# Kernel tuning notes

Measured on AMD Instinct MI355X. Metric: run time of the kernel, lower is better.

Reference implementation:

```python
import jax, jax.numpy as jnp
import numpy as np

N, E = 50000, 800000
IN, HID, OUT, K = 500, 128, 128, 10
BN_EPS = 1e-5


def _encode(x, src, dst, norm, n, W_in, b_in, gam, high_pass, bn_scale, bn_shift, W_up, b_up):
    # input projection (dropout_p = 0 -> identity)
    h = x @ W_in + b_in  # [N, HID]

    def prop(t):
        # symmetric-normalized sparse matvec: (D^-1/2 A D^-1/2) t
        return jax.ops.segment_sum(norm[:, None] * t[src], dst, num_segments=n)

    def step(carry, g):
        t, acc = carry
        acc = acc + g * t
        pt = prop(t)
        # low-pass basis: A_hat^k x ; high-pass basis: (I - A_hat)^k x
        t = (t - pt) if high_pass else pt
        return (t, acc), None

    (_, acc), _ = jax.lax.scan(step, (h, jnp.zeros_like(h)), gam)

    # BatchNorm1d over the node axis (training-mode batch statistics)
    mu = acc.mean(axis=0)
    var = acc.var(axis=0)
    hn = (acc - mu) * jax.lax.rsqrt(var + BN_EPS) * bn_scale + bn_shift
    z = hn @ W_up + b_up
    return jax.nn.relu(z)  # act_fn='relu' (PolyGCL default)


def setup_inputs() -> dict:
    key = jax.random.key(0)
    ks = jax.random.split(key, 4)
    x = jax.random.normal(ks[0], (N, IN), dtype=jnp.float32)
    edge_index = jax.random.randint(ks[1], (2, E), 0, N, dtype=jnp.int32)
    W_in = jax.random.normal(ks[2], (IN, HID), dtype=jnp.float32) * (1.0 / np.sqrt(IN))
    b_in = jnp.zeros((HID,), dtype=jnp.float32)
    # low-pass: decreasing coefficients; high-pass: increasing (PolyGCL init scheme)
    gamma_L = jnp.linspace(2.0, 0.0, K + 1, dtype=jnp.float32)
    gamma_H = jnp.linspace(0.0, 2.0, K + 1, dtype=jnp.float32)
    bn_scale = jnp.ones((HID,), dtype=jnp.float32)
    bn_shift = jnp.zeros((HID,), dtype=jnp.float32)
    W_up = jax.random.normal(ks[3], (HID, OUT), dtype=jnp.float32) * (1.0 / np.sqrt(HID))
    b_up = jnp.zeros((OUT,), dtype=jnp.float32)
    return {"x": x, "edge_index": edge_index, "W_in": W_in, "b_in": b_in,
            "gamma_L": gamma_L, "gamma_H": gamma_H,
            "bn_scale": bn_scale, "bn_shift": bn_shift,
            "W_up": W_up, "b_up": b_up}


def reference(x, edge_index, W_in, b_in, gamma_L, gamma_H, bn_scale, bn_shift, W_up, b_up):
    n = x.shape[0]
    src, dst = edge_index[0], edge_index[1]
    deg = jax.ops.segment_sum(jnp.ones(src.shape, dtype=x.dtype), dst, num_segments=n)
    dinv = jax.lax.rsqrt(jnp.maximum(deg, 1.0))
    norm = dinv[src] * dinv[dst]  # [E]
    Z_L = _encode(x, src, dst, norm, n, W_in, b_in, gamma_L, False, bn_scale, bn_shift, W_up, b_up)
    Z_H = _encode(x, src, dst, norm, n, W_in, b_in, gamma_H, True, bn_scale, bn_shift, W_up, b_up)
    return (Z_L, Z_H)
```

## Files before the change

kernel.cpp:

```cpp
#include <hip/hip_runtime.h>
#include <hip/hip_fp16.h>

#define HIDF 128

typedef float v4f __attribute__((ext_vector_type(4)));
typedef _Float16 half8 __attribute__((ext_vector_type(8)));
typedef float f32x4 __attribute__((ext_vector_type(4)));
struct alignas(8) half4 { __half2 lo, hi; };

static inline int cdiv(int a, int b) { return (a + b - 1) / b; }
static inline size_t alup(size_t b) { return (b + 255) & ~(size_t)255; }

__global__ void k_deg(const int* __restrict__ dst, int E, int* __restrict__ deg) {
    int i = blockIdx.x * blockDim.x + threadIdx.x;
    if (i < E) atomicAdd(&deg[dst[i]], 1);
}

__global__ void k_coef(const float* __restrict__ gL, const float* __restrict__ gH, int K,
                       float* __restrict__ cL, float* __restrict__ cH) {
    if (threadIdx.x == 0 && blockIdx.x == 0) {
        for (int j = 0; j <= K; ++j) {
            double s = 0.0;
            double C = 1.0;
            for (int k = j; k <= K; ++k) {
                s += (double)gH[k] * C;
                C = C * (double)(k + 1) / (double)(k + 1 - j);
            }
            cH[j] = (j & 1) ? (float)(-s) : (float)s;
            cL[j] = gL[j];
        }
    }
}

__global__ __launch_bounds__(256) void k_scan1(const int* __restrict__ deg, int N,
                                               int* __restrict__ bsum,
                                               float* __restrict__ dinv) {
    __shared__ int ls[256];
    int tid = threadIdx.x;
    int i = blockIdx.x * 256 + tid;
    int v = 0;
    if (i < N) {
        v = deg[i];
        dinv[i] = rsqrtf(fmaxf((float)v, 1.0f));
    }
    ls[tid] = v;
    __syncthreads();
    for (int off = 128; off > 0; off >>= 1) {
        if (tid < off) ls[tid] += ls[tid + off];
        __syncthreads();
    }
    if (tid == 0) bsum[blockIdx.x] = ls[0];
}

__global__ __launch_bounds__(1024) void k_scan2(int* __restrict__ bsum, int nb) {
    __shared__ int ls[1024];
    int tid = threadIdx.x;
    int v = (tid < nb) ? bsum[tid] : 0;
    ls[tid] = v;
    __syncthreads();
    for (int off = 1; off < 1024; off <<= 1) {
        int t = (tid >= off) ? ls[tid - off] : 0;
        __syncthreads();
        ls[tid] += t;
        __syncthreads();
    }
    if (tid < nb) bsum[tid] = ls[tid] - v;
}

__global__ __launch_bounds__(256) void k_scan3(const int* __restrict__ deg,
                                               const int* __restrict__ bsum, int N,
                                               int* __restrict__ row_ptr) {
    __shared__ int ls[256];
    int tid = threadIdx.x;
    int i = blockIdx.x * 256 + tid;
    int v = (i < N) ? deg[i] : 0;
    ls[tid] = v;
    __syncthreads();
    for (int off = 1; off < 256; off <<= 1) {
        int t = (tid >= off) ? ls[tid - off] : 0;
        __syncthreads();
        ls[tid] += t;
        __syncthreads();
    }
    if (i <= N) row_ptr[i] = bsum[blockIdx.x] + ls[tid] - v;
}

__global__ __launch_bounds__(1024) void k_scan(const int* __restrict__ deg, int N,
                                               int* __restrict__ row_ptr,
                                               float* __restrict__ dinv) {
    __shared__ int ls[1024];
    int tid = threadIdx.x;
    int chunk = (N + 1023) / 1024;
    int start = tid * chunk;
    int end = min(start + chunk, N);
    int s = 0;
    for (int i = start; i < end; ++i) {
        int d = deg[i];
        s += d;
        dinv[i] = rsqrtf(fmaxf((float)d, 1.0f));
    }
    ls[tid] = s;
    __syncthreads();
    for (int off = 1; off < 1024; off <<= 1) {
        int v = (tid >= off) ? ls[tid - off] : 0;
        __syncthreads();
        ls[tid] += v;
        __syncthreads();
    }
    int run = ls[tid] - s;
    for (int i = start; i < end; ++i) {
        row_ptr[i] = run;
        run += deg[i];
    }
    if (tid == 1023) row_ptr[N] = run;
}

__global__ void k_scatter(const int* __restrict__ src, const int* __restrict__ dst, int E,
                          const int* __restrict__ row_ptr, int* __restrict__ fill,
                          const float* __restrict__ dinv, int* __restrict__ csr_src,
                          float* __restrict__ csr_w) {
    int i = blockIdx.x * blockDim.x + threadIdx.x;
    if (i < E) {
        int s = src[i], d = dst[i];
        int pos = row_ptr[d] + atomicAdd(&fill[d], 1);
        csr_src[pos] = s;
        csr_w[pos] = dinv[s] * dinv[d];
    }
}

__global__ __launch_bounds__(512) void k_wprep(const float* __restrict__ W, int Kdim, int KP,
                                               _Float16* __restrict__ Wh,
                                               _Float16* __restrict__ Wl) {
    int i = blockIdx.x * blockDim.x + threadIdx.x;
    int total = 128 * KP;
    if (i >= total) return;
    int n = i / KP;
    int k = i - n * KP;
    float w = (k < Kdim) ? W[(long)k * HIDF + n] : 0.0f;
    _Float16 h = (_Float16)w;
    _Float16 l = (_Float16)(w - (float)h);
    Wh[(long)n * KP + k] = h;
    Wl[(long)n * KP + k] = l;
}

__global__ __launch_bounds__(512) void k_gemm_in_mfma(
    const float* __restrict__ X, const _Float16* __restrict__ Wh,
    const _Float16* __restrict__ Wl, const float* __restrict__ b, __half* __restrict__ U0,
    int M, int Kdim, int KP) {
    __shared__ _Float16 Apk[64][64];
    __shared__ _Float16 Bpk[128][64];
    int tid = threadIdx.x;
    int lane = tid & 63;
    int wid = tid >> 6;
    int wr = wid >> 1;
    int wc = wid & 1;
    int lr = lane & 15;
    int kq = lane >> 4;
    int row0 = blockIdx.x * 64;
    int sm = tid >> 2;
    int ks = tid & 3;
    int kk = ks * 8;
    bool k4ok = ((Kdim & 3) == 0);

    f32x4 acc[4] = {};

    for (int k0 = 0; k0 < KP; k0 += 32) {
        {
            half8 wbh = *(const half8*)&Wh[(long)sm * KP + k0 + kk];
            half8 wbl = *(const half8*)&Wl[(long)sm * KP + k0 + kk];
            int sw = sm & 7;
            *(half8*)&Bpk[sm][(ks ^ sw) << 3] = wbh;
            *(half8*)&Bpk[sm][((ks | 4) ^ sw) << 3] = wbl;
        }
        if (tid < 256) {
            int r = row0 + sm;
            int gk = k0 + kk;
            half8 hv, lv;
            if (r < M && k4ok && (gk + 8) <= Kdim) {
                float4 v0 = *(const float4*)&X[(long)r * Kdim + gk];
                float4 v1 = *(const float4*)&X[(long)r * Kdim + gk + 4];
                float xs[8] = {v0.x, v0.y, v0.z, v0.w, v1.x, v1.y, v1.z, v1.w};
#pragma unroll
                for (int j = 0; j < 8; ++j) {
                    _Float16 h = (_Float16)xs[j];
                    hv[j] = h;
                    lv[j] = (_Float16)(xs[j] - (float)h);
                }
            } else {
#pragma unroll
                for (int j = 0; j < 8; ++j) {
                    float x = (r < M && (gk + j) < Kdim) ? X[(long)r * Kdim + gk + j] : 0.0f;
                    _Float16 h = (_Float16)x;
                    hv[j] = h;
                    lv[j] = (_Float16)(x - (float)h);
                }
            }
            int sw = sm & 7;
            *(half8*)&Apk[sm][(ks ^ sw) << 3] = hv;
            *(half8*)&Apk[sm][((ks | 4) ^ sw) << 3] = lv;
        }
        __syncthreads();

        int ra = wr * 16 + lr;
        int swa = ra & 7;
        half8 a_h = *(const half8*)&Apk[ra][(kq ^ swa) << 3];
        half8 a_l = *(const half8*)&Apk[ra][((kq | 4) ^ swa) << 3];
#pragma unroll
        for (int cg = 0; cg < 4; ++cg) {
            int rb = wc * 64 + cg * 16 + lr;
            int swb = rb & 7;
            half8 b_h = *(const half8*)&Bpk[rb][(kq ^ swb) << 3];
            half8 b_l = *(const half8*)&Bpk[rb][((kq | 4) ^ swb) << 3];
            acc[cg] = __builtin_amdgcn_mfma_f32_16x16x32_f16(a_h, b_h, acc[cg], 0, 0, 0);
            acc[cg] = __builtin_amdgcn_mfma_f32_16x16x32_f16(a_l, b_h, acc[cg], 0, 0, 0);
            acc[cg] = __builtin_amdgcn_mfma_f32_16x16x32_f16(a_h, b_l, acc[cg], 0, 0, 0);
        }
        __syncthreads();
    }

    float bb[4];
#pragma unroll
    for (int cg = 0; cg < 4; ++cg) bb[cg] = b[wc * 64 + cg * 16 + lr];
#pragma unroll
    for (int j = 0; j < 4; ++j) {
        int r = row0 + wr * 16 + kq * 4 + j;
        if (r < M) {
#pragma unroll
            for (int cg = 0; cg < 4; ++cg) {
                int n = wc * 64 + cg * 16 + lr;
                U0[(long)r * HIDF + n] = __float2half(acc[cg][j] + bb[cg]);
            }
        }
    }
}

__global__ __launch_bounds__(512) void k_gemm_up_mfma(
    const float* __restrict__ accL, const float* __restrict__ accH,
    const _Float16* __restrict__ Wh, const _Float16* __restrict__ Wl,
    const float* __restrict__ bias, const float* __restrict__ a_mul,
    const float* __restrict__ aaW, float* __restrict__ out, int M) {
    int enc = blockIdx.y;
    const float* A = enc ? accH : accL;
    float* O = out + (size_t)enc * M * HIDF;
    __shared__ _Float16 Apk[128][64];
    __shared__ _Float16 Bpk[128][64];
    __shared__ float ams[128];
    int tid = threadIdx.x;
    int lane = tid & 63;
    int wid = tid >> 6;
    int wr = wid >> 1;
    int wc = wid & 1;
    int lr = lane & 15;
    int kq = lane >> 4;
    int row0 = blockIdx.x * 128;
    int sm = tid >> 2;
    int ks = tid & 3;
    int kk = ks * 8;
    if (tid < 128) ams[tid] = a_mul[enc * 128 + tid];
    __syncthreads();

    f32x4 acc[2][4] = {};

    for (int k0 = 0; k0 < 128; k0 += 32) {
        {
            half8 wbh = *(const half8*)&Wh[(long)sm * 128 + k0 + kk];
            half8 wbl = *(const half8*)&Wl[(long)sm * 128 + k0 + kk];
            int sw = sm & 7;
            *(half8*)&Bpk[sm][(ks ^ sw) << 3] = wbh;
            *(half8*)&Bpk[sm][((ks | 4) ^ sw) << 3] = wbl;
        }
        {
            int r = row0 + sm;
            half8 hv, lv;
            if (r < M) {
                float4 v0 = *(const float4*)&A[(long)r * 128 + k0 + kk];
                float4 v1 = *(const float4*)&A[(long)r * 128 + k0 + kk + 4];
                float xs[8] = {v0.x, v0.y, v0.z, v0.w, v1.x, v1.y, v1.z, v1.w};
#pragma unroll
                for (int j = 0; j < 8; ++j) {
                    float sv = xs[j] * ams[k0 + kk + j];
                    _Float16 h = (_Float16)sv;
                    hv[j] = h;
                    lv[j] = (_Float16)(sv - (float)h);
                }
            } else {
#pragma unroll
                for (int j = 0; j < 8; ++j) { hv[j] = (_Float16)0.f; lv[j] = (_Float16)0.f; }
            }
            int sw = sm & 7;
            *(half8*)&Apk[sm][(ks ^ sw) << 3] = hv;
            *(half8*)&Apk[sm][((ks | 4) ^ sw) << 3] = lv;
        }
        __syncthreads();

        int ra0 = wr * 32 + lr;
        int ra1 = wr * 32 + 16 + lr;
        int swa0 = ra0 & 7, swa1 = ra1 & 7;
        half8 a_h0 = *(const half8*)&Apk[ra0][(kq ^ swa0) << 3];
        half8 a_h1 = *(const half8*)&Apk[ra1][(kq ^ swa1) << 3];
        half8 a_l0 = *(const half8*)&Apk[ra0][((kq | 4) ^ swa0) << 3];
        half8 a_l1 = *(const half8*)&Apk[ra1][((kq | 4) ^ swa1) << 3];
#pragma unroll
        for (int cg = 0; cg < 4; ++cg) {
            int rb = wc * 64 + cg * 16 + lr;
            int swb = rb & 7;
            half8 b_h = *(const half8*)&Bpk[rb][(kq ^ swb) << 3];
            half8 b_l = *(const half8*)&Bpk[rb][((kq | 4) ^ swb) << 3];
            acc[0][cg] = __builtin_amdgcn_mfma_f32_16x16x32_f16(a_h0, b_h, acc[0][cg], 0, 0, 0);
            acc[1][cg] = __builtin_amdgcn_mfma_f32_16x16x32_f16(a_h1, b_h, acc[1][cg], 0, 0, 0);
            acc[0][cg] = __builtin_amdgcn_mfma_f32_16x16x32_f16(a_l0, b_h, acc[0][cg], 0, 0, 0);
            acc[1][cg] = __builtin_amdgcn_mfma_f32_16x16x32_f16(a_l1, b_h, acc[1][cg], 0, 0, 0);
            acc[0][cg] = __builtin_amdgcn_mfma_f32_16x16x32_f16(a_h0, b_l, acc[0][cg], 0, 0, 0);
            acc[1][cg] = __builtin_amdgcn_mfma_f32_16x16x32_f16(a_h1, b_l, acc[1][cg], 0, 0, 0);
        }
        __syncthreads();
    }

    float bb[4];
#pragma unroll
    for (int cg = 0; cg < 4; ++cg) {
        int n = wc * 64 + cg * 16 + lr;
        bb[cg] = bias[n] + aaW[enc * 128 + n];
    }
#pragma unroll
    for (int i = 0; i < 2; ++i) {
#pragma unroll
        for (int j = 0; j < 4; ++j) {
            int r = row0 + wr * 32 + i * 16 + kq * 4 + j;
            if (r < M) {
#pragma unroll
                for (int cg = 0; cg < 4; ++cg) {
                    int n = wc * 64 + cg * 16 + lr;
                    O[(long)r * HIDF + n] = fmaxf(acc[i][cg][j] + bb[cg], 0.0f);
                }
            }
        }
    }
}

__global__ __launch_bounds__(512) void k_gemm_in_f(
    const float* __restrict__ X, const float* __restrict__ W, const float* __restrict__ b,
    float* __restrict__ H, float* __restrict__ accL, float* __restrict__ accH,
    const float* __restrict__ cL, const float* __restrict__ cH, int M, int Kdim) {
    const int BK = 20;
    __shared__ float As[BK][132];
    __shared__ float Bs[BK][128];
    int tid = threadIdx.x;
    int tx = tid & 31, ty = tid >> 5;
    int row0 = blockIdx.x * 128;
    float acc[8][4] = {};
    for (int k0 = 0; k0 < Kdim; k0 += BK) {
        for (int l = tid; l < 640; l += 512) {
            int m = l / 5, q = l % 5;
            int r = row0 + m;
            float4 v = {0.f, 0.f, 0.f, 0.f};
            if (r < M) v = *(const float4*)&X[(long)r * Kdim + k0 + q * 4];
            As[q * 4 + 0][m] = v.x;
            As[q * 4 + 1][m] = v.y;
            As[q * 4 + 2][m] = v.z;
            As[q * 4 + 3][m] = v.w;
        }
        for (int l = tid; l < 640; l += 512) {
            int k = l >> 5, n = (l & 31) * 4;
            *(float4*)&Bs[k][n] = *(const float4*)&W[(long)(k0 + k) * 128 + n];
        }
        __syncthreads();
#pragma unroll
        for (int k = 0; k < BK; ++k) {
            float4 a0 = *(const float4*)&As[k][ty * 8];
            float4 a1 = *(const float4*)&As[k][ty * 8 + 4];
            float4 bb = *(const float4*)&Bs[k][tx * 4];
            float a[8] = {a0.x, a0.y, a0.z, a0.w, a1.x, a1.y, a1.z, a1.w};
#pragma unroll
            for (int i = 0; i < 8; ++i) {
                acc[i][0] += a[i] * bb.x;
                acc[i][1] += a[i] * bb.y;
                acc[i][2] += a[i] * bb.z;
                acc[i][3] += a[i] * bb.w;
            }
        }
        __syncthreads();
    }
    float g0 = cL[0], h0 = cH[0];
    float4 bias = *(const float4*)&b[tx * 4];
    float bv[4] = {bias.x, bias.y, bias.z, bias.w};
#pragma unroll
    for (int i = 0; i < 8; ++i) {
        int r = row0 + ty * 8 + i;
        if (r < M) {
            long idx = (long)r * 128 + tx * 4;
            float4 vh;
            float* ph = (float*)&vh;
#pragma unroll
            for (int j = 0; j < 4; ++j) ph[j] = acc[i][j] + bv[j];
            *(float4*)&H[idx] = vh;
            float4 vl = {g0 * vh.x, g0 * vh.y, g0 * vh.z, g0 * vh.w};
            float4 vv = {h0 * vh.x, h0 * vh.y, h0 * vh.z, h0 * vh.w};
            *(float4*)&accL[idx] = vl;
            *(float4*)&accH[idx] = vv;
        }
    }
}

__global__ __launch_bounds__(256) void k_prop_h(
    const int* __restrict__ row_ptr, const int* __restrict__ csr_src,
    const float* __restrict__ csr_w, const __half* __restrict__ t_in,
    __half* __restrict__ t_out, int N) {
    int wave = threadIdx.x >> 6;
    int lane = threadIdx.x & 63;
    int half = lane >> 5;
    int l5 = lane & 31;
    int node = blockIdx.x * 4 + wave;
    if (node >= N) return;
    int e0 = row_ptr[node], e1 = row_ptr[node + 1];
    float sx = 0.f, sy = 0.f, sz = 0.f, sw = 0.f;
    int e = e0 + half;
    for (; e + 14 < e1; e += 16) {
        int idx[8];
        float w[8];
        half4 v[8];
#pragma unroll
        for (int q = 0; q < 8; ++q) {
            idx[q] = csr_src[e + 2 * q];
            w[q] = csr_w[e + 2 * q];
        }
#pragma unroll
        for (int q = 0; q < 8; ++q) v[q] = *(const half4*)&t_in[(long)idx[q] * HIDF + l5 * 4];
#pragma unroll
        for (int q = 0; q < 8; ++q) {
            float2 a = __half22float2(v[q].lo), b2 = __half22float2(v[q].hi);
            sx += w[q] * a.x;
            sy += w[q] * a.y;
            sz += w[q] * b2.x;
            sw += w[q] * b2.y;
        }
    }
    for (; e + 6 < e1; e += 8) {
        int idx[4];
        float w[4];
        half4 v[4];
#pragma unroll
        for (int q = 0; q < 4; ++q) {
            idx[q] = csr_src[e + 2 * q];
            w[q] = csr_w[e + 2 * q];
        }
#pragma unroll
        for (int q = 0; q < 4; ++q) v[q] = *(const half4*)&t_in[(long)idx[q] * HIDF + l5 * 4];
#pragma unroll
        for (int q = 0; q < 4; ++q) {
            float2 a = __half22float2(v[q].lo), b2 = __half22float2(v[q].hi);
            sx += w[q] * a.x;
            sy += w[q] * a.y;
            sz += w[q] * b2.x;
            sw += w[q] * b2.y;
        }
    }
    for (; e < e1; e += 2) {
        int i0 = csr_src[e];
        float w0 = csr_w[e];
        half4 v0 = *(const half4*)&t_in[(long)i0 * HIDF + l5 * 4];
        float2 a0 = __half22float2(v0.lo), b0 = __half22float2(v0.hi);
        sx += w0 * a0.x;
        sy += w0 * a0.y;
        sz += w0 * b0.x;
        sw += w0 * b0.y;
    }
    sx += __shfl_xor(sx, 32);
    sy += __shfl_xor(sy, 32);
    sz += __shfl_xor(sz, 32);
    sw += __shfl_xor(sw, 32);
    if (half == 0) {
        half4 o;
        o.lo = __float22half2_rn(make_float2(sx, sy));
        o.hi = __float22half2_rn(make_float2(sz, sw));
        *(half4*)&t_out[(long)node * HIDF + l5 * 4] = o;
    }
}

__global__ __launch_bounds__(256) void k_prop(
    const int* __restrict__ row_ptr, const int* __restrict__ csr_src,
    const float* __restrict__ csr_w, const float* __restrict__ t_in,
    float* __restrict__ t_out, float* __restrict__ accL, float* __restrict__ accH,
    const float* __restrict__ cL, const float* __restrict__ cH, int j, int N, int write_t) {
    int wave = threadIdx.x >> 6;
    int lane = threadIdx.x & 63;
    int half = lane >> 5;
    int l5 = lane & 31;
    int node = blockIdx.x * 4 + wave;
    if (node >= N) return;
    int e0 = row_ptr[node], e1 = row_ptr[node + 1];
    float sx = 0.f, sy = 0.f, sz = 0.f, sw = 0.f;
    int e = e0 + half;
    for (; e + 6 < e1; e += 8) {
        int i0 = csr_src[e], i1 = csr_src[e + 2], i2 = csr_src[e + 4], i3 = csr_src[e + 6];
        float w0 = csr_w[e], w1 = csr_w[e + 2], w2 = csr_w[e + 4], w3 = csr_w[e + 6];
        float4 v0 = *(const float4*)&t_in[(long)i0 * HIDF + l5 * 4];
        float4 v1 = *(const float4*)&t_in[(long)i1 * HIDF + l5 * 4];
        float4 v2 = *(const float4*)&t_in[(long)i2 * HIDF + l5 * 4];
        float4 v3 = *(const float4*)&t_in[(long)i3 * HIDF + l5 * 4];
        sx += w0 * v0.x + w1 * v1.x + w2 * v2.x + w3 * v3.x;
        sy += w0 * v0.y + w1 * v1.y + w2 * v2.y + w3 * v3.y;
        sz += w0 * v0.z + w1 * v1.z + w2 * v2.z + w3 * v3.z;
        sw += w0 * v0.w + w1 * v1.w + w2 * v2.w + w3 * v3.w;
    }
    for (; e < e1; e += 2) {
        int i0 = csr_src[e];
        float w0 = csr_w[e];
        float4 v0 = *(const float4*)&t_in[(long)i0 * HIDF + l5 * 4];
        sx += w0 * v0.x;
        sy += w0 * v0.y;
        sz += w0 * v0.z;
        sw += w0 * v0.w;
    }
    sx += __shfl_xor(sx, 32);
    sy += __shfl_xor(sy, 32);
    sz += __shfl_xor(sz, 32);
    sw += __shfl_xor(sw, 32);
    if (half == 0) {
        long base = (long)node * HIDF + l5 * 4;
        if (write_t) {
            float4 o = {sx, sy, sz, sw};
            *(float4*)&t_out[base] = o;
        }
        float gL = cL[j], gH = cH[j];
        float4 aL = *(const float4*)&accL[base];
        float4 aH = *(const float4*)&accH[base];
        aL.x += gL * sx; aL.y += gL * sy; aL.z += gL * sz; aL.w += gL * sw;
        aH.x += gH * sx; aH.y += gH * sy; aH.z += gH * sz; aH.w += gH * sw;
        *(float4*)&accL[base] = aL;
        *(float4*)&accH[base] = aH;
    }
}

__global__ __launch_bounds__(256) void k_combine_h2(
    const __half* __restrict__ tb, long tstride, int K, float* __restrict__ accL,
    float* __restrict__ accH, const float* __restrict__ cL, const float* __restrict__ cH,
    int N, float* __restrict__ sums) {
    int tid = threadIdx.x;
    int fg = tid & 15;
    int rg = tid >> 4;
    int lane = tid & 63;
    int wid = tid >> 6;
    float s1[8] = {}, s2[8] = {}, s3[8] = {}, s4[8] = {};

    if (K == 10) {
        float gl[11], gh[11];
#pragma unroll
        for (int j = 0; j < 11; ++j) {
            gl[j] = cL[j];
            gh[j] = cH[j];
        }
        for (long r = (long)blockIdx.x * 16 + rg; r < N; r += (long)gridDim.x * 16) {
            const __half* p = tb + r * HIDF + fg * 8;
            half8 v[11];
#pragma unroll
            for (int j = 0; j < 11; ++j) v[j] = *(const half8*)(p + (long)j * tstride);
            float aL[8] = {}, aH[8] = {};
#pragma unroll
            for (int j = 0; j < 11; ++j) {
#pragma unroll
                for (int e = 0; e < 8; ++e) {
                    float t = (float)v[j][e];
                    aL[e] += gl[j] * t;
                    aH[e] += gh[j] * t;
                }
            }
            long base = r * HIDF + fg * 8;
            float4 o0 = {aL[0], aL[1], aL[2], aL[3]};
            float4 o1 = {aL[4], aL[5], aL[6], aL[7]};
            float4 o2 = {aH[0], aH[1], aH[2], aH[3]};
            float4 o3 = {aH[4], aH[5], aH[6], aH[7]};
            *(float4*)&accL[base] = o0;
            *(float4*)&accL[base + 4] = o1;
            *(float4*)&accH[base] = o2;
            *(float4*)&accH[base + 4] = o3;
#pragma unroll
            for (int e = 0; e < 8; ++e) {
                s1[e] += aL[e];
                s2[e] += aL[e] * aL[e];
                s3[e] += aH[e];
                s4[e] += aH[e] * aH[e];
            }
        }
    } else {
        for (long r = (long)blockIdx.x * 16 + rg; r < N; r += (long)gridDim.x * 16) {
            const __half* p = tb + r * HIDF + fg * 8;
            float aL[8] = {}, aH[8] = {};
            for (int j = 0; j <= K; ++j) {
                half8 v = *(const half8*)(p + (long)j * tstride);
                float gL = cL[j], gH = cH[j];
#pragma unroll
                for (int e = 0; e < 8; ++e) {
                    float t = (float)v[e];
                    aL[e] += gL * t;
                    aH[e] += gH * t;
                }
            }
            long base = r * HIDF + fg * 8;
            float4 o0 = {aL[0], aL[1], aL[2], aL[3]};
            float4 o1 = {aL[4], aL[5], aL[6], aL[7]};
            float4 o2 = {aH[0], aH[1], aH[2], aH[3]};
            float4 o3 = {aH[4], aH[5], aH[6], aH[7]};
            *(float4*)&accL[base] = o0;
            *(float4*)&accL[base + 4] = o1;
            *(float4*)&accH[base] = o2;
            *(float4*)&accH[base + 4] = o3;
#pragma unroll
            for (int e = 0; e < 8; ++e) {
                s1[e] += aL[e];
                s2[e] += aL[e] * aL[e];
                s3[e] += aH[e];
                s4[e] += aH[e] * aH[e];
            }
        }
    }

#pragma unroll
    for (int e = 0; e < 8; ++e) {
        s1[e] += __shfl_xor(s1[e], 16); s1[e] += __shfl_xor(s1[e], 32);
        s2[e] += __shfl_xor(s2[e], 16); s2[e] += __shfl_xor(s2[e], 32);
        s3[e] += __shfl_xor(s3[e], 16); s3[e] += __shfl_xor(s3[e], 32);
        s4[e] += __shfl_xor(s4[e], 16); s4[e] += __shfl_xor(s4[e], 32);
    }
    __shared__ float ls[4][16][32];
    if (lane < 16) {
#pragma unroll
        for (int e = 0; e < 8; ++e) {
            ls[wid][lane][e] = s1[e];
            ls[wid][lane][8 + e] = s2[e];
            ls[wid][lane][16 + e] = s3[e];
            ls[wid][lane][24 + e] = s4[e];
        }
    }
    __syncthreads();
    for (int idx = tid; idx < 512; idx += 256) {
        int f16i = idx >> 5, j = idx & 31;
        float v = ls[0][f16i][j] + ls[1][f16i][j] + ls[2][f16i][j] + ls[3][f16i][j];
        int stat = j >> 3, e = j & 7;
        atomicAdd(&sums[stat * 128 + f16i * 8 + e], v);
    }
}

__global__ __launch_bounds__(256) void k_stats(const float* __restrict__ accL,
                                               const float* __restrict__ accH, int N,
                                               float* __restrict__ sums) {
    int tid = threadIdx.x;
    int l5 = tid & 31;
    int g = tid >> 5;
    float4 l1 = {0, 0, 0, 0}, l2 = {0, 0, 0, 0}, h1 = {0, 0, 0, 0}, h2 = {0, 0, 0, 0};
    for (int r = blockIdx.x * 8 + g; r < N; r += gridDim.x * 8) {
        float4 v = *(const float4*)&accL[(long)r * HIDF + l5 * 4];
        l1.x += v.x; l1.y += v.y; l1.z += v.z; l1.w += v.w;
        l2.x += v.x * v.x; l2.y += v.y * v.y; l2.z += v.z * v.z; l2.w += v.w * v.w;
        float4 u = *(const float4*)&accH[(long)r * HIDF + l5 * 4];
        h1.x += u.x; h1.y += u.y; h1.z += u.z; h1.w += u.w;
        h2.x += u.x * u.x; h2.y += u.y * u.y; h2.z += u.z * u.z; h2.w += u.w * u.w;
    }
    __shared__ float4 s1[256], s2[256], s3[256], s4[256];
    s1[tid] = l1; s2[tid] = l2; s3[tid] = h1; s4[tid] = h2;
    __syncthreads();
    if (tid < 32) {
        float4 a = s1[tid], bq = s2[tid], c = s3[tid], d = s4[tid];
        for (int gg = 1; gg < 8; ++gg) {
            float4 t;
            t = s1[gg * 32 + tid]; a.x += t.x; a.y += t.y; a.z += t.z; a.w += t.w;
            t = s2[gg * 32 + tid]; bq.x += t.x; bq.y += t.y; bq.z += t.z; bq.w += t.w;
            t = s3[gg * 32 + tid]; c.x += t.x; c.y += t.y; c.z += t.z; c.w += t.w;
            t = s4[gg * 32 + tid]; d.x += t.x; d.y += t.y; d.z += t.z; d.w += t.w;
        }
        int f = tid * 4;
        atomicAdd(&sums[f + 0], a.x); atomicAdd(&sums[f + 1], a.y);
        atomicAdd(&sums[f + 2], a.z); atomicAdd(&sums[f + 3], a.w);
        atomicAdd(&sums[128 + f + 0], bq.x); atomicAdd(&sums[128 + f + 1], bq.y);
        atomicAdd(&sums[128 + f + 2], bq.z); atomicAdd(&sums[128 + f + 3], bq.w);
        atomicAdd(&sums[256 + f + 0], c.x); atomicAdd(&sums[256 + f + 1], c.y);
        atomicAdd(&sums[256 + f + 2], c.z); atomicAdd(&sums[256 + f + 3], c.w);
        atomicAdd(&sums[384 + f + 0], d.x); atomicAdd(&sums[384 + f + 1], d.y);
        atomicAdd(&sums[384 + f + 2], d.z); atomicAdd(&sums[384 + f + 3], d.w);
    }
}

__global__ void k_bnfin(const float* __restrict__ sums, int N, const float* __restrict__ scale,
                        const float* __restrict__ shift, const float* __restrict__ Wup,
                        float* __restrict__ a_mul, float* __restrict__ a_add,
                        float* __restrict__ aaW) {
    __shared__ float sh_add[2][128];
    int f = threadIdx.x;
    for (int enc = 0; enc < 2; ++enc) {
        float mu = sums[enc * 256 + f] / (float)N;
        float var = sums[enc * 256 + 128 + f] / (float)N - mu * mu;
        float rstd = rsqrtf(var + 1e-5f);
        float am = rstd * scale[f];
        a_mul[enc * 128 + f] = am;
        float ad = shift[f] - mu * am;
        a_add[enc * 128 + f] = ad;
        sh_add[enc][f] = ad;
    }
    __syncthreads();
    int n = f;
    float s0 = 0.f, s1 = 0.f;
    for (int ff = 0; ff < 128; ++ff) {
        float w = Wup[ff * 128 + n];
        s0 += sh_add[0][ff] * w;
        s1 += sh_add[1][ff] * w;
    }
    aaW[n] = s0;
    aaW[128 + n] = s1;
}

extern "C" void kernel_launch(void* const* d_in, const int* in_sizes, int n_in, void* d_out,
                              int out_size, void* d_ws, size_t ws_size, hipStream_t stream) {
    const float* x = (const float*)d_in[0];
    const int* edge_index = (const int*)d_in[1];
    const float* W_in = (const float*)d_in[2];
    const float* b_in = (const float*)d_in[3];
    const float* gamma_L = (const float*)d_in[4];
    const float* gamma_H = (const float*)d_in[5];
    const float* bn_scale = (const float*)d_in[6];
    const float* bn_shift = (const float*)d_in[7];
    const float* W_up = (const float*)d_in[8];
    const float* b_up = (const float*)d_in[9];
    float* out = (float*)d_out;

    const int HID = in_sizes[3];
    const int IN = in_sizes[2] / HID;
    const int N = in_sizes[0] / IN;
    const int E = in_sizes[1] / 2;
    const int K = in_sizes[4] - 1;

    const int* src = edge_index;
    const int* dst = edge_index + E;

    const int KP = (IN + 31) & ~31;

    char* base = (char*)d_ws;
    size_t off = 0;
    auto take = [&](size_t bytes) -> char* {
        char* r = base + off;
        off += alup(bytes);
        return r;
    };
    int* deg = (int*)take((size_t)N * 4);
    int* row_ptr = (int*)take((size_t)(N + 1) * 4);
    int* fill = (int*)take((size_t)N * 4);
    float* dinv = (float*)take((size_t)N * 4);
    int* bsum = (int*)take(1024 * 4);
    int* csr_src = (int*)take((size_t)E * 4);
    float* csr_w = (float*)take((size_t)E * 4);
    float* accL = (float*)take((size_t)N * HID * 4);
    float* accH = (float*)take((size_t)N * HID * 4);
    float* sums = (float*)take(512 * 4);
    float* cL = (float*)take(64 * 4);
    float* cH = (float*)take(64 * 4);
    float* a_mul = (float*)take(256 * 4);
    float* a_add = (float*)take(256 * 4);
    float* aaW = (float*)take(256 * 4);
    _Float16* Wt_h = (_Float16*)take((size_t)HID * KP * 2);
    _Float16* Wt_l = (_Float16*)take((size_t)HID * KP * 2);
    _Float16* Wup_h = (_Float16*)take((size_t)HID * HID * 2);
    _Float16* Wup_l = (_Float16*)take((size_t)HID * HID * 2);

    size_t per16 = alup((size_t)N * HID * 2);
    long stride16 = (long)(per16 / 2);
    __half* tb16 = (__half*)(base + off);
    bool deferred = (off + (size_t)(K + 1) * per16) <= ws_size && K < 60 && (HID == 128);
    size_t per32 = alup((size_t)N * HID * 4);
    long stride32 = (long)(per32 / 4);
    float* fb = (float*)(base + off);

    hipMemsetAsync(deg, 0, (size_t)N * 4, stream);
    hipMemsetAsync(fill, 0, (size_t)N * 4, stream);
    hipMemsetAsync(sums, 0, 512 * 4, stream);

    k_coef<<<1, 64, 0, stream>>>(gamma_L, gamma_H, K, cL, cH);
    k_deg<<<cdiv(E, 256), 256, 0, stream>>>(dst, E, deg);

    int nb = cdiv(N + 1, 256);
    if (nb <= 1024) {
        k_scan1<<<nb, 256, 0, stream>>>(deg, N, bsum, dinv);
        k_scan2<<<1, 1024, 0, stream>>>(bsum, nb);
        k_scan3<<<nb, 256, 0, stream>>>(deg, bsum, N, row_ptr);
    } else {
        k_scan<<<1, 1024, 0, stream>>>(deg, N, row_ptr, dinv);
    }

    k_scatter<<<cdiv(E, 256), 256, 0, stream>>>(src, dst, E, row_ptr, fill, dinv, csr_src,
                                                csr_w);
    k_wprep<<<cdiv(HID * HID, 512), 512, 0, stream>>>(W_up, HID, HID, Wup_h, Wup_l);

    if (deferred) {
        k_wprep<<<cdiv(HID * KP, 512), 512, 0, stream>>>(W_in, IN, KP, Wt_h, Wt_l);
        k_gemm_in_mfma<<<cdiv(N, 64), 512, 0, stream>>>(x, Wt_h, Wt_l, b_in, tb16, N, IN, KP);
        for (int j = 1; j <= K; ++j) {
            const __half* tin = tb16 + (long)(j - 1) * stride16;
            __half* tout = tb16 + (long)j * stride16;
            k_prop_h<<<cdiv(N, 4), 256, 0, stream>>>(row_ptr, csr_src, csr_w, tin, tout, N);
        }
        k_combine_h2<<<512, 256, 0, stream>>>(tb16, stride16, K, accL, accH, cL, cH, N, sums);
    } else {
        float* h = fb;
        float* ta = fb + stride32;
        k_gemm_in_f<<<cdiv(N, 128), 512, 0, stream>>>(x, W_in, b_in, h, accL, accH, cL, cH,
                                                      N, IN);
        const float* tin = h;
        float* tout = ta;
        for (int j = 1; j <= K; ++j) {
            int write_t = (j < K) ? 1 : 0;
            k_prop<<<cdiv(N, 4), 256, 0, stream>>>(row_ptr, csr_src, csr_w, tin, tout, accL,
                                                   accH, cL, cH, j, N, write_t);
            const float* nt = tout;
            tout = (nt == ta) ? h : ta;
            tin = nt;
        }
        k_stats<<<200, 256, 0, stream>>>(accL, accH, N, sums);
    }

    k_bnfin<<<1, 128, 0, stream>>>(sums, N, bn_scale, bn_shift, W_up, a_mul, a_add, aaW);
    dim3 gup(cdiv(N, 128), 2);
    k_gemm_up_mfma<<<gup, 512, 0, stream>>>(accL, accH, Wup_h, Wup_l, b_up, a_mul, aaW, out,
                                            N);
}
```

Before: 691.2 us.

## Double input GEMM row tile, rework LDS swizzle, use nontemporal CSR loads

The input-projection MFMA GEMM now computes 128 rows per block instead of 64, so all 512 threads load A and each B fragment is reused across two A fragments. Both GEMMs switch to a new LDS slot swizzle (hslot) meant to reduce bank conflicts. The half-precision propagation kernel reads CSR indices and weights with nontemporal loads and writes outputs with nontemporal stores, so the streaming edge data is less likely to evict gathered features from cache. The trade-off is more registers and LDS per block, and fewer blocks for the 50k-row GEMM.

```diff
diff --git a/kernel.cpp b/kernel.cpp
--- a/kernel.cpp
+++ b/kernel.cpp
@@ -10,6 +10,10 @@
 
 static inline int cdiv(int a, int b) { return (a + b - 1) / b; }
 static inline size_t alup(size_t b) { return (b + 255) & ~(size_t)255; }
+
+__device__ __forceinline__ int hslot(int k, int r) {
+    return (k ^ ((r >> 1) & 3)) | ((r & 1) << 2);
+}
 
 __global__ void k_deg(const int* __restrict__ dst, int E, int* __restrict__ deg) {
     int i = blockIdx.x * blockDim.x + threadIdx.x;
@@ -147,7 +151,7 @@
     const float* __restrict__ X, const _Float16* __restrict__ Wh,
     const _Float16* __restrict__ Wl, const float* __restrict__ b, __half* __restrict__ U0,
     int M, int Kdim, int KP) {
-    __shared__ _Float16 Apk[64][64];
+    __shared__ _Float16 Apk[128][64];
     __shared__ _Float16 Bpk[128][64];
     int tid = threadIdx.x;
     int lane = tid & 63;
@@ -156,23 +160,23 @@
     int wc = wid & 1;
     int lr = lane & 15;
     int kq = lane >> 4;
-    int row0 = blockIdx.x * 64;
+    int row0 = blockIdx.x * 128;
     int sm = tid >> 2;
     int ks = tid & 3;
     int kk = ks * 8;
     bool k4ok = ((Kdim & 3) == 0);
 
-    f32x4 acc[4] = {};
+    f32x4 acc[2][4] = {};
 
     for (int k0 = 0; k0 < KP; k0 += 32) {
+        int swh = hslot(ks, sm);
         {
             half8 wbh = *(const half8*)&Wh[(long)sm * KP + k0 + kk];
             half8 wbl = *(const half8*)&Wl[(long)sm * KP + k0 + kk];
-            int sw = sm & 7;
-            *(half8*)&Bpk[sm][(ks ^ sw) << 3] = wbh;
-            *(half8*)&Bpk[sm][((ks | 4) ^ sw) << 3] = wbl;
-        }
-        if (tid < 256) {
+            *(half8*)&Bpk[sm][swh << 3] = wbh;
+            *(half8*)&Bpk[sm][(swh ^ 4) << 3] = wbl;
+        }
+        {
             int r = row0 + sm;
             int gk = k0 + kk;
             half8 hv, lv;
@@ -195,25 +199,30 @@
                     lv[j] = (_Float16)(x - (float)h);
                 }
             }
-            int sw = sm & 7;
-            *(half8*)&Apk[sm][(ks ^ sw) << 3] = hv;
-            *(half8*)&Apk[sm][((ks | 4) ^ sw) << 3] = lv;
-        }
-        __syncthreads();
-
-        int ra = wr * 16 + lr;
-        int swa = ra & 7;
-        half8 a_h = *(const half8*)&Apk[ra][(kq ^ swa) << 3];
-        half8 a_l = *(const half8*)&Apk[ra][((kq | 4) ^ swa) << 3];
+            *(half8*)&Apk[sm][swh << 3] = hv;
+            *(half8*)&Apk[sm][(swh ^ 4) << 3] = lv;
+        }
+        __syncthreads();
+
+        int ra0 = wr * 32 + lr;
+        int ra1 = wr * 32 + 16 + lr;
+        int sa0 = hslot(kq, ra0), sa1 = hslot(kq, ra1);
+        half8 a_h0 = *(const half8*)&Apk[ra0][sa0 << 3];
+        half8 a_h1 = *(const half8*)&Apk[ra1][sa1 << 3];
+        half8 a_l0 = *(const half8*)&Apk[ra0][(sa0 ^ 4) << 3];
+        half8 a_l1 = *(const half8*)&Apk[ra1][(sa1 ^ 4) << 3];
 #pragma unroll
         for (int cg = 0; cg < 4; ++cg) {
             int rb = wc * 64 + cg * 16 + lr;
-            int swb = rb & 7;
-            half8 b_h = *(const half8*)&Bpk[rb][(kq ^ swb) << 3];
-            half8 b_l = *(const half8*)&Bpk[rb][((kq | 4) ^ swb) << 3];
-            acc[cg] = __builtin_amdgcn_mfma_f32_16x16x32_f16(a_h, b_h, acc[cg], 0, 0, 0);
-            acc[cg] = __builtin_amdgcn_mfma_f32_16x16x32_f16(a_l, b_h, acc[cg], 0, 0, 0);
-            acc[cg] = __builtin_amdgcn_mfma_f32_16x16x32_f16(a_h, b_l, acc[cg], 0, 0, 0);
+            int sb = hslot(kq, rb);
+            half8 b_h = *(const half8*)&Bpk[rb][sb << 3];
+            half8 b_l = *(const half8*)&Bpk[rb][(sb ^ 4) << 3];
+            acc[0][cg] = __builtin_amdgcn_mfma_f32_16x16x32_f16(a_h0, b_h, acc[0][cg], 0, 0, 0);
+            acc[1][cg] = __builtin_amdgcn_mfma_f32_16x16x32_f16(a_h1, b_h, acc[1][cg], 0, 0, 0);
+            acc[0][cg] = __builtin_amdgcn_mfma_f32_16x16x32_f16(a_l0, b_h, acc[0][cg], 0, 0, 0);
+            acc[1][cg] = __builtin_amdgcn_mfma_f32_16x16x32_f16(a_l1, b_h, acc[1][cg], 0, 0, 0);
+            acc[0][cg] = __builtin_amdgcn_mfma_f32_16x16x32_f16(a_h0, b_l, acc[0][cg], 0, 0, 0);
+            acc[1][cg] = __builtin_amdgcn_mfma_f32_16x16x32_f16(a_h1, b_l, acc[1][cg], 0, 0, 0);
         }
         __syncthreads();
     }
@@ -222,13 +231,16 @@
 #pragma unroll
     for (int cg = 0; cg < 4; ++cg) bb[cg] = b[wc * 64 + cg * 16 + lr];
 #pragma unroll
-    for (int j = 0; j < 4; ++j) {
-        int r = row0 + wr * 16 + kq * 4 + j;
-        if (r < M) {
-#pragma unroll
-            for (int cg = 0; cg < 4; ++cg) {
-                int n = wc * 64 + cg * 16 + lr;
-                U0[(long)r * HIDF + n] = __float2half(acc[cg][j] + bb[cg]);
+    for (int i = 0; i < 2; ++i) {
+#pragma unroll
+        for (int j = 0; j < 4; ++j) {
+            int r = row0 + wr * 32 + i * 16 + kq * 4 + j;
+            if (r < M) {
+#pragma unroll
+                for (int cg = 0; cg < 4; ++cg) {
+                    int n = wc * 64 + cg * 16 + lr;
+                    U0[(long)r * HIDF + n] = __float2half(acc[i][cg][j] + bb[cg]);
+                }
             }
         }
     }
@@ -262,12 +274,12 @@
     f32x4 acc[2][4] = {};
 
     for (int k0 = 0; k0 < 128; k0 += 32) {
+        int swh = hslot(ks, sm);
         {
             half8 wbh = *(const half8*)&Wh[(long)sm * 128 + k0 + kk];
             half8 wbl = *(const half8*)&Wl[(long)sm * 128 + k0 + kk];
-            int sw = sm & 7;
-            *(half8*)&Bpk[sm][(ks ^ sw) << 3] = wbh;
-            *(half8*)&Bpk[sm][((ks | 4) ^ sw) << 3] = wbl;
+            *(half8*)&Bpk[sm][swh << 3] = wbh;
+            *(half8*)&Bpk[sm][(swh ^ 4) << 3] = wbl;
         }
         {
             int r = row0 + sm;
@@ -287,25 +299,24 @@
 #pragma unroll
                 for (int j = 0; j < 8; ++j) { hv[j] = (_Float16)0.f; lv[j] = (_Float16)0.f; }
             }
-            int sw = sm & 7;
-            *(half8*)&Apk[sm][(ks ^ sw) << 3] = hv;
-            *(half8*)&Apk[sm][((ks | 4) ^ sw) << 3] = lv;
+            *(half8*)&Apk[sm][swh << 3] = hv;
+            *(half8*)&Apk[sm][(swh ^ 4) << 3] = lv;
         }
         __syncthreads();
 
         int ra0 = wr * 32 + lr;
         int ra1 = wr * 32 + 16 + lr;
-        int swa0 = ra0 & 7, swa1 = ra1 & 7;
-        half8 a_h0 = *(const half8*)&Apk[ra0][(kq ^ swa0) << 3];
-        half8 a_h1 = *(const half8*)&Apk[ra1][(kq ^ swa1) << 3];
-        half8 a_l0 = *(const half8*)&Apk[ra0][((kq | 4) ^ swa0) << 3];
-        half8 a_l1 = *(const half8*)&Apk[ra1][((kq | 4) ^ swa1) << 3];
+        int sa0 = hslot(kq, ra0), sa1 = hslot(kq, ra1);
+        half8 a_h0 = *(const half8*)&Apk[ra0][sa0 << 3];
+        half8 a_h1 = *(const half8*)&Apk[ra1][sa1 << 3];
+        half8 a_l0 = *(const half8*)&Apk[ra0][(sa0 ^ 4) << 3];
+        half8 a_l1 = *(const half8*)&Apk[ra1][(sa1 ^ 4) << 3];
 #pragma unroll
         for (int cg = 0; cg < 4; ++cg) {
             int rb = wc * 64 + cg * 16 + lr;
-            int swb = rb & 7;
-            half8 b_h = *(const half8*)&Bpk[rb][(kq ^ swb) << 3];
-            half8 b_l = *(const half8*)&Bpk[rb][((kq | 4) ^ swb) << 3];
+            int sb = hslot(kq, rb);
+            half8 b_h = *(const half8*)&Bpk[rb][sb << 3];
+            half8 b_l = *(const half8*)&Bpk[rb][(sb ^ 4) << 3];
             acc[0][cg] = __builtin_amdgcn_mfma_f32_16x16x32_f16(a_h0, b_h, acc[0][cg], 0, 0, 0);
             acc[1][cg] = __builtin_amdgcn_mfma_f32_16x16x32_f16(a_h1, b_h, acc[1][cg], 0, 0, 0);
             acc[0][cg] = __builtin_amdgcn_mfma_f32_16x16x32_f16(a_l0, b_h, acc[0][cg], 0, 0, 0);
@@ -421,8 +432,8 @@
         half4 v[8];
 #pragma unroll
         for (int q = 0; q < 8; ++q) {
-            idx[q] = csr_src[e + 2 * q];
-            w[q] = csr_w[e + 2 * q];
+            idx[q] = __builtin_nontemporal_load(&csr_src[e + 2 * q]);
+            w[q] = __builtin_nontemporal_load(&csr_w[e + 2 * q]);
         }
 #pragma unroll
         for (int q = 0; q < 8; ++q) v[q] = *(const half4*)&t_in[(long)idx[q] * HIDF + l5 * 4];
@@ -441,8 +452,8 @@
         half4 v[4];
 #pragma unroll
         for (int q = 0; q < 4; ++q) {
-            idx[q] = csr_src[e + 2 * q];
-            w[q] = csr_w[e + 2 * q];
+            idx[q] = __builtin_nontemporal_load(&csr_src[e + 2 * q]);
+            w[q] = __builtin_nontemporal_load(&csr_w[e + 2 * q]);
         }
 #pragma unroll
         for (int q = 0; q < 4; ++q) v[q] = *(const half4*)&t_in[(long)idx[q] * HIDF + l5 * 4];
@@ -456,8 +467,8 @@
         }
     }
     for (; e < e1; e += 2) {
-        int i0 = csr_src[e];
-        float w0 = csr_w[e];
+        int i0 = __builtin_nontemporal_load(&csr_src[e]);
+        float w0 = __builtin_nontemporal_load(&csr_w[e]);
         half4 v0 = *(const half4*)&t_in[(long)i0 * HIDF + l5 * 4];
         float2 a0 = __half22float2(v0.lo), b0 = __half22float2(v0.hi);
         sx += w0 * a0.x;
@@ -473,7 +484,8 @@
         half4 o;
         o.lo = __float22half2_rn(make_float2(sx, sy));
         o.hi = __float22half2_rn(make_float2(sz, sw));
-        *(half4*)&t_out[(long)node * HIDF + l5 * 4] = o;
+        __builtin_nontemporal_store(*(long long*)&o,
+                                    (long long*)&t_out[(long)node * HIDF + l5 * 4]);
     }
 }
 
@@ -790,7 +802,7 @@
 
     if (deferred) {
         k_wprep<<<cdiv(HID * KP, 512), 512, 0, stream>>>(W_in, IN, KP, Wt_h, Wt_l);
-        k_gemm_in_mfma<<<cdiv(N, 64), 512, 0, stream>>>(x, Wt_h, Wt_l, b_in, tb16, N, IN, KP);
+        k_gemm_in_mfma<<<cdiv(N, 128), 512, 0, stream>>>(x, Wt_h, Wt_l, b_in, tb16, N, IN, KP);
         for (int j = 1; j <= K; ++j) {
             const __half* tin = tb16 + (long)(j - 1) * stride16;
             __half* tout = tb16 + (long)j * stride16;
```

Measured after the change: 770.8 us. 11.5% more time.
